# Kernel optimization log

Measured on AMD Instinct MI355X. Metric: run time of the kernel, lower is better.

Reference implementation:

```python
import jax, jax.numpy as jnp
import numpy as np

N = 16384          # num_nodes
B = 2              # batch_size
F = 32             # feature_size (hard-coded in module)
G = 16             # num_gru_units
OUT = 16           # output_dim


def _normalized_laplacian(adj):
    # calculate_laplacian_with_self_loop: D^-1/2 (A + I) D^-1/2
    a = adj + jnp.eye(adj.shape[0], dtype=adj.dtype)
    d = a.sum(axis=1)
    dinv = jax.lax.rsqrt(d)
    return dinv[:, None] * a * dinv[None, :]


def setup_inputs() -> dict:
    key = jax.random.key(0)
    k1, k2, k3, k4 = jax.random.split(key, 4)
    adj = (jax.random.uniform(k1, (N, N), dtype=jnp.float32) < 0.01).astype(jnp.float32)
    laplacian = _normalized_laplacian(adj)
    inputs = jax.random.normal(k2, (B, N, F), dtype=jnp.float32)
    hidden_state = jax.random.normal(k3, (B, N * G), dtype=jnp.float32)
    # xavier_uniform for weights [(G+F), OUT]
    limit = np.sqrt(6.0 / (G + F + OUT)).astype(np.float32)
    weights = jax.random.uniform(k4, (G + F, OUT), dtype=jnp.float32, minval=-limit, maxval=limit)
    biases = jnp.zeros((OUT,), dtype=jnp.float32)
    return {"inputs": inputs, "hidden_state": hidden_state, "laplacian": laplacian,
            "weights": weights, "biases": biases}


def reference(inputs, hidden_state, laplacian, weights, biases):
    b, n, f = inputs.shape
    g = weights.shape[0] - f
    out_dim = weights.shape[1]
    h = hidden_state.reshape(b, n, g)
    cat = jnp.concatenate([inputs, h], axis=2)              # [B, N, F+G]
    # laplacian @ concat over the node dimension (same math as the
    # reshape/transpose dance + per-batch sparse GEMM loop in the original)
    ax = jnp.einsum('mn,bnc->bmc', laplacian, cat)          # [B, N, F+G]
    out = ax @ weights + biases                             # [B, N, OUT]
    return out.reshape(b, n * out_dim)
```

## Files before the change

kernel.cpp:

```cpp
#include <hip/hip_runtime.h>
#include <hip/hip_bf16.h>


#define NN   16384
#define FF   32
#define GG   16
#define OUTD 16
#define C96  96
#define BM   64
#define BK   64
#define SPLITK 4
#define KCHUNK (NN / SPLITK)
#define KITERS (KCHUNK / BK)

typedef __attribute__((ext_vector_type(8))) short short8;
typedef __attribute__((ext_vector_type(4))) float f32x4;

using as1_void = __attribute__((address_space(1))) void;
using as3_void = __attribute__((address_space(3))) void;

__device__ __forceinline__ unsigned short f2bf(float f) {
  __hip_bfloat16 h = __float2bfloat16(f);
  return __builtin_bit_cast(unsigned short, h);
}

__global__ __launch_bounds__(256) void prep_xt(const float* __restrict__ inp,
                                               const float* __restrict__ hid,
                                               unsigned short* __restrict__ xt) {
  __shared__ float lds_cat[C96][64];
  const int tid = threadIdx.x;
  const int n0 = blockIdx.x * 64;

#pragma unroll
  for (int r = 0; r < 2; ++r) {
    int fi = tid + r * 256;
    int n = fi >> 3;
    int f4 = fi & 7;
#pragma unroll
    for (int b = 0; b < 2; ++b) {
      const float4* src = (const float4*)(inp + ((size_t)b * NN + (n0 + n)) * FF) + f4;
      float4 v = *src;
      int c = b * 48 + f4 * 4;
      lds_cat[c + 0][n] = v.x;
      lds_cat[c + 1][n] = v.y;
      lds_cat[c + 2][n] = v.z;
      lds_cat[c + 3][n] = v.w;
    }
  }
  {
    int n = tid >> 2;
    int g4 = tid & 3;
#pragma unroll
    for (int b = 0; b < 2; ++b) {
      const float4* src = (const float4*)(hid + ((size_t)b * NN + (n0 + n)) * GG) + g4;
      float4 v = *src;
      int c = b * 48 + 32 + g4 * 4;
      lds_cat[c + 0][n] = v.x;
      lds_cat[c + 1][n] = v.y;
      lds_cat[c + 2][n] = v.z;
      lds_cat[c + 3][n] = v.w;
    }
  }
  __syncthreads();
#pragma unroll
  for (int r = 0; r < 3; ++r) {
    int u = tid + r * 256;
    int c = u >> 3;
    int nn = (u & 7) * 8;
    short8 o;
#pragma unroll
    for (int j = 0; j < 8; ++j) o[j] = (short)f2bf(lds_cat[c][nn + j]);
    *(short8*)(xt + (size_t)c * NN + n0 + nn) = o;
  }
}

__global__ __launch_bounds__(256, 4) void spmm_main(const float* __restrict__ L,
                                                    const unsigned short* __restrict__ xt,
                                                    float* __restrict__ cp) {
  __shared__ __align__(16) float lds_a[BM * BK];
  __shared__ __align__(16) unsigned short lds_b[C96 * BK];

  const int tid = threadIdx.x;
  const int wave = tid >> 6;
  const int lane = tid & 63;
  const int m0 = blockIdx.x * BM;
  const int kbase = blockIdx.y * KCHUNK;

  const float* asrc[4];
  float* adst[4];
#pragma unroll
  for (int a = 0; a < 4; ++a) {
    int s = wave * 256 + a * 64 + lane;
    int row = s >> 4;
    int cu = (s & 15) ^ (row & 15);
    asrc[a] = L + (size_t)(m0 + row) * NN + kbase + cu * 4;
    adst[a] = lds_a + (wave * 256 + a * 64) * 4;
  }
  const unsigned short* bsrc[3];
  unsigned short* bdst[3];
#pragma unroll
  for (int bi = 0; bi < 3; ++bi) {
    int s = wave * 192 + bi * 64 + lane;
    int c = s >> 3;
    int kg = (s & 7) ^ (c & 7);
    bsrc[bi] = xt + (size_t)c * NN + kbase + kg * 8;
    bdst[bi] = lds_b + (wave * 192 + bi * 64) * 8;
  }

  const int rowA = wave * 16 + (lane & 15);
  const int lq = lane >> 4;
  int aoff[2][2];
#pragma unroll
  for (int kk = 0; kk < 2; ++kk) {
    int cu0 = kk * 8 + lq * 2;
    aoff[kk][0] = (rowA * 16 + (cu0 ^ (rowA & 15))) * 4;
    aoff[kk][1] = (rowA * 16 + ((cu0 + 1) ^ (rowA & 15))) * 4;
  }
  int boff[2][6];
#pragma unroll
  for (int kk = 0; kk < 2; ++kk)
#pragma unroll
    for (int t = 0; t < 6; ++t) {
      int c = t * 16 + (lane & 15);
      int kg = kk * 4 + lq;
      boff[kk][t] = (c * 8 + (kg ^ (c & 7))) * 8;
    }

  f32x4 acc[6];
#pragma unroll
  for (int t = 0; t < 6; ++t) acc[t] = (f32x4){0.f, 0.f, 0.f, 0.f};

  for (int it = 0; it < KITERS; ++it) {
    const int ko = it * BK;
#pragma unroll
    for (int a = 0; a < 4; ++a)
      __builtin_amdgcn_global_load_lds((const as1_void*)(asrc[a] + ko),
                                       (as3_void*)adst[a], 16, 0, 0);
#pragma unroll
    for (int bi = 0; bi < 3; ++bi)
      __builtin_amdgcn_global_load_lds((const as1_void*)(bsrc[bi] + ko),
                                       (as3_void*)bdst[bi], 16, 0, 0);
    __syncthreads();

#pragma unroll
    for (int kk = 0; kk < 2; ++kk) {
      f32x4 a0 = *(const f32x4*)(lds_a + aoff[kk][0]);
      f32x4 a1 = *(const f32x4*)(lds_a + aoff[kk][1]);
      short8 af;
      af[0] = (short)f2bf(a0[0]);
      af[1] = (short)f2bf(a0[1]);
      af[2] = (short)f2bf(a0[2]);
      af[3] = (short)f2bf(a0[3]);
      af[4] = (short)f2bf(a1[0]);
      af[5] = (short)f2bf(a1[1]);
      af[6] = (short)f2bf(a1[2]);
      af[7] = (short)f2bf(a1[3]);
#pragma unroll
      for (int t = 0; t < 6; ++t) {
        short8 bf = *(const short8*)(lds_b + boff[kk][t]);
        acc[t] = __builtin_amdgcn_mfma_f32_16x16x32_bf16(af, bf, acc[t], 0, 0, 0);
      }
    }
    __syncthreads();
  }

  float* cpd = cp + ((size_t)blockIdx.y * NN + m0) * C96;
#pragma unroll
  for (int t = 0; t < 6; ++t) {
    int col = t * 16 + (lane & 15);
#pragma unroll
    for (int r = 0; r < 4; ++r) {
      int row = wave * 16 + lq * 4 + r;
      cpd[(size_t)row * C96 + col] = acc[t][r];
    }
  }
}

__global__ __launch_bounds__(256) void epilogue(const float* __restrict__ cp,
                                                const float* __restrict__ w,
                                                const float* __restrict__ bias,
                                                float* __restrict__ out) {
  __shared__ float lds_c[64 * 97];
  __shared__ float lds_w[48 * 16];
  __shared__ float lds_bias[16];
  const int tid = threadIdx.x;
  const int n0 = blockIdx.x * 64;

  for (int i = tid; i < 768; i += 256) lds_w[i] = w[i];
  if (tid < 16) lds_bias[tid] = bias[tid];

  const size_t base = (size_t)n0 * C96;
#pragma unroll
  for (int i = 0; i < 24; ++i) {
    int e = tid + i * 256;
    float s = 0.f;
#pragma unroll
    for (int sp = 0; sp < 4; ++sp)
      s += cp[(size_t)sp * (NN * C96) + base + e];
    lds_c[e + e / 96] = s;
  }
  __syncthreads();

  const int node = tid >> 2;
  const int b = (tid >> 1) & 1;
  const int o0 = (tid & 1) * 8;
  const float* crow = &lds_c[node * 97 + b * 48];
  float accv[8];
#pragma unroll
  for (int o = 0; o < 8; ++o) accv[o] = lds_bias[o0 + o];
#pragma unroll
  for (int j = 0; j < 48; ++j) {
    float cv = crow[j];
#pragma unroll
    for (int o = 0; o < 8; ++o) accv[o] += cv * lds_w[j * 16 + o0 + o];
  }
  size_t ob = (size_t)b * (NN * OUTD) + (size_t)(n0 + node) * OUTD + o0;
  float4 v0 = {accv[0], accv[1], accv[2], accv[3]};
  float4 v1 = {accv[4], accv[5], accv[6], accv[7]};
  *(float4*)(out + ob) = v0;
  *(float4*)(out + ob + 4) = v1;
}

extern "C" void kernel_launch(void* const* d_in, const int* in_sizes, int n_in,
                              void* d_out, int out_size, void* d_ws, size_t ws_size,
                              hipStream_t stream) {
  (void)in_sizes; (void)n_in; (void)out_size; (void)ws_size;
  const float* inp = (const float*)d_in[0];
  const float* hid = (const float*)d_in[1];
  const float* lap = (const float*)d_in[2];
  const float* wts = (const float*)d_in[3];
  const float* bia = (const float*)d_in[4];
  float* out = (float*)d_out;

  unsigned short* xt = (unsigned short*)d_ws;
  float* cp = (float*)((char*)d_ws + (4u << 20));

  prep_xt<<<NN / 64, 256, 0, stream>>>(inp, hid, xt);
  spmm_main<<<dim3(NN / BM, SPLITK), 256, 0, stream>>>(lap, xt, cp);
  epilogue<<<NN / 64, 256, 0, stream>>>(cp, wts, bia, out);
}
```

Before: 1.343 ms.

## Double-buffer LDS tiles in SpMM main loop and halve split-K with block swizzle

Result: no change. 1.330 ms (-1.0%).

```diff
diff --git a/kernel.cpp b/kernel.cpp
--- a/kernel.cpp
+++ b/kernel.cpp
@@ -9,7 +9,7 @@
 #define C96  96
 #define BM   64
 #define BK   64
-#define SPLITK 4
+#define SPLITK 2
 #define KCHUNK (NN / SPLITK)
 #define KITERS (KCHUNK / BK)
 
@@ -22,6 +22,12 @@
 __device__ __forceinline__ unsigned short f2bf(float f) {
   __hip_bfloat16 h = __float2bfloat16(f);
   return __builtin_bit_cast(unsigned short, h);
+}
+
+__device__ __forceinline__ void wg_barrier() {
+  asm volatile("" ::: "memory");
+  __builtin_amdgcn_s_barrier();
+  asm volatile("" ::: "memory");
 }
 
 __global__ __launch_bounds__(256) void prep_xt(const float* __restrict__ inp,
@@ -74,37 +80,42 @@
   }
 }
 
-__global__ __launch_bounds__(256, 4) void spmm_main(const float* __restrict__ L,
+__global__ __launch_bounds__(256, 2) void spmm_main(const float* __restrict__ L,
                                                     const unsigned short* __restrict__ xt,
                                                     float* __restrict__ cp) {
-  __shared__ __align__(16) float lds_a[BM * BK];
-  __shared__ __align__(16) unsigned short lds_b[C96 * BK];
+  __shared__ __align__(16) float lds_a[2][BM * BK];
+  __shared__ __align__(16) unsigned short lds_b[2][C96 * BK];
 
   const int tid = threadIdx.x;
   const int wave = tid >> 6;
   const int lane = tid & 63;
-  const int m0 = blockIdx.x * BM;
-  const int kbase = blockIdx.y * KCHUNK;
+
+  const int wg = blockIdx.x;
+  const int swz = (wg & 7) * (512 / 8) + (wg >> 3);
+  const int my = swz >> 8;
+  const int mx = swz & 255;
+  const int m0 = mx * BM;
+  const int kbase = my * KCHUNK;
 
   const float* asrc[4];
-  float* adst[4];
+  int adst[4];
 #pragma unroll
   for (int a = 0; a < 4; ++a) {
     int s = wave * 256 + a * 64 + lane;
     int row = s >> 4;
     int cu = (s & 15) ^ (row & 15);
     asrc[a] = L + (size_t)(m0 + row) * NN + kbase + cu * 4;
-    adst[a] = lds_a + (wave * 256 + a * 64) * 4;
+    adst[a] = (wave * 256 + a * 64) * 4;
   }
   const unsigned short* bsrc[3];
-  unsigned short* bdst[3];
+  int bdst[3];
 #pragma unroll
   for (int bi = 0; bi < 3; ++bi) {
     int s = wave * 192 + bi * 64 + lane;
     int c = s >> 3;
     int kg = (s & 7) ^ (c & 7);
     bsrc[bi] = xt + (size_t)c * NN + kbase + kg * 8;
-    bdst[bi] = lds_b + (wave * 192 + bi * 64) * 8;
+    bdst[bi] = (wave * 192 + bi * 64) * 8;
   }
 
   const int rowA = wave * 16 + (lane & 15);
@@ -130,22 +141,22 @@
 #pragma unroll
   for (int t = 0; t < 6; ++t) acc[t] = (f32x4){0.f, 0.f, 0.f, 0.f};
 
-  for (int it = 0; it < KITERS; ++it) {
-    const int ko = it * BK;
+  auto stage = [&](int buf, int ko) {
 #pragma unroll
     for (int a = 0; a < 4; ++a)
       __builtin_amdgcn_global_load_lds((const as1_void*)(asrc[a] + ko),
-                                       (as3_void*)adst[a], 16, 0, 0);
+                                       (as3_void*)(&lds_a[buf][adst[a]]), 16, 0, 0);
 #pragma unroll
     for (int bi = 0; bi < 3; ++bi)
       __builtin_amdgcn_global_load_lds((const as1_void*)(bsrc[bi] + ko),
-                                       (as3_void*)bdst[bi], 16, 0, 0);
-    __syncthreads();
-
+                                       (as3_void*)(&lds_b[buf][bdst[bi]]), 16, 0, 0);
+  };
+
+  auto compute = [&](int buf) {
 #pragma unroll
     for (int kk = 0; kk < 2; ++kk) {
-      f32x4 a0 = *(const f32x4*)(lds_a + aoff[kk][0]);
-      f32x4 a1 = *(const f32x4*)(lds_a + aoff[kk][1]);
+      f32x4 a0 = *(const f32x4*)(&lds_a[buf][aoff[kk][0]]);
+      f32x4 a1 = *(const f32x4*)(&lds_a[buf][aoff[kk][1]]);
       short8 af;
       af[0] = (short)f2bf(a0[0]);
       af[1] = (short)f2bf(a0[1]);
@@ -157,14 +168,29 @@
       af[7] = (short)f2bf(a1[3]);
 #pragma unroll
       for (int t = 0; t < 6; ++t) {
-        short8 bf = *(const short8*)(lds_b + boff[kk][t]);
+        short8 bf = *(const short8*)(&lds_b[buf][boff[kk][t]]);
         acc[t] = __builtin_amdgcn_mfma_f32_16x16x32_bf16(af, bf, acc[t], 0, 0, 0);
       }
     }
-    __syncthreads();
-  }
-
-  float* cpd = cp + ((size_t)blockIdx.y * NN + m0) * C96;
+  };
+
+  stage(0, 0);
+  int cur = 0;
+  for (int it = 0; it < KITERS - 1; ++it) {
+    stage(cur ^ 1, (it + 1) * BK);
+    asm volatile("s_waitcnt vmcnt(7)" ::: "memory");
+    __builtin_amdgcn_s_barrier();
+    asm volatile("" ::: "memory");
+    compute(cur);
+    wg_barrier();
+    cur ^= 1;
+  }
+  asm volatile("s_waitcnt vmcnt(0)" ::: "memory");
+  __builtin_amdgcn_s_barrier();
+  asm volatile("" ::: "memory");
+  compute(cur);
+
+  float* cpd = cp + ((size_t)my * NN + m0) * C96;
 #pragma unroll
   for (int t = 0; t < 6; ++t) {
     int col = t * 16 + (lane & 15);
@@ -195,7 +221,7 @@
     int e = tid + i * 256;
     float s = 0.f;
 #pragma unroll
-    for (int sp = 0; sp < 4; ++sp)
+    for (int sp = 0; sp < SPLITK; ++sp)
       s += cp[(size_t)sp * (NN * C96) + base + e];
     lds_c[e + e / 96] = s;
   }
@@ -236,6 +262,6 @@
   float* cp = (float*)((char*)d_ws + (4u << 20));
 
   prep_xt<<<NN / 64, 256, 0, stream>>>(inp, hid, xt);
-  spmm_main<<<dim3(NN / BM, SPLITK), 256, 0, stream>>>(lap, xt, cp);
+  spmm_main<<<dim3(NN / BM * SPLITK), 256, 0, stream>>>(lap, xt, cp);
   epilogue<<<NN / 64, 256, 0, stream>>>(cp, wts, bia, out);
 }
```

## Load SpMM operands directly from global into registers with prefetch and block swizzle

Applied to the files above, without the earlier changes.

After: 1.533 ms. 14.1% more time.

```diff
diff --git a/kernel.cpp b/kernel.cpp
--- a/kernel.cpp
+++ b/kernel.cpp
@@ -12,12 +12,10 @@
 #define SPLITK 4
 #define KCHUNK (NN / SPLITK)
 #define KITERS (KCHUNK / BK)
+#define NWG   (NN / BM * SPLITK)
 
 typedef __attribute__((ext_vector_type(8))) short short8;
 typedef __attribute__((ext_vector_type(4))) float f32x4;
-
-using as1_void = __attribute__((address_space(1))) void;
-using as3_void = __attribute__((address_space(3))) void;
 
 __device__ __forceinline__ unsigned short f2bf(float f) {
   __hip_bfloat16 h = __float2bfloat16(f);
@@ -77,75 +75,50 @@
 __global__ __launch_bounds__(256, 4) void spmm_main(const float* __restrict__ L,
                                                     const unsigned short* __restrict__ xt,
                                                     float* __restrict__ cp) {
-  __shared__ __align__(16) float lds_a[BM * BK];
-  __shared__ __align__(16) unsigned short lds_b[C96 * BK];
-
   const int tid = threadIdx.x;
   const int wave = tid >> 6;
   const int lane = tid & 63;
-  const int m0 = blockIdx.x * BM;
-  const int kbase = blockIdx.y * KCHUNK;
-
-  const float* asrc[4];
-  float* adst[4];
-#pragma unroll
-  for (int a = 0; a < 4; ++a) {
-    int s = wave * 256 + a * 64 + lane;
-    int row = s >> 4;
-    int cu = (s & 15) ^ (row & 15);
-    asrc[a] = L + (size_t)(m0 + row) * NN + kbase + cu * 4;
-    adst[a] = lds_a + (wave * 256 + a * 64) * 4;
-  }
-  const unsigned short* bsrc[3];
-  unsigned short* bdst[3];
-#pragma unroll
-  for (int bi = 0; bi < 3; ++bi) {
-    int s = wave * 192 + bi * 64 + lane;
-    int c = s >> 3;
-    int kg = (s & 7) ^ (c & 7);
-    bsrc[bi] = xt + (size_t)c * NN + kbase + kg * 8;
-    bdst[bi] = lds_b + (wave * 192 + bi * 64) * 8;
-  }
-
-  const int rowA = wave * 16 + (lane & 15);
   const int lq = lane >> 4;
-  int aoff[2][2];
-#pragma unroll
-  for (int kk = 0; kk < 2; ++kk) {
-    int cu0 = kk * 8 + lq * 2;
-    aoff[kk][0] = (rowA * 16 + (cu0 ^ (rowA & 15))) * 4;
-    aoff[kk][1] = (rowA * 16 + ((cu0 + 1) ^ (rowA & 15))) * 4;
-  }
-  int boff[2][6];
+  const int lr = lane & 15;
+
+  const int wg = blockIdx.x;
+  const int swz = (wg & 7) * (NWG / 8) + (wg >> 3);
+  const int my = swz >> 8;
+  const int mx = swz & 255;
+  const int m0 = mx * BM;
+  const int kbase = my * KCHUNK;
+
+  const float* arow = L + (size_t)(m0 + wave * 16 + lr) * NN + kbase + lq * 8;
+  const unsigned short* bb0 = xt + (size_t)(0 * 16 + lr) * NN + kbase + lq * 8;
+  const unsigned short* bb1 = xt + (size_t)(1 * 16 + lr) * NN + kbase + lq * 8;
+  const unsigned short* bb2 = xt + (size_t)(2 * 16 + lr) * NN + kbase + lq * 8;
+  const unsigned short* bb3 = xt + (size_t)(3 * 16 + lr) * NN + kbase + lq * 8;
+  const unsigned short* bb4 = xt + (size_t)(4 * 16 + lr) * NN + kbase + lq * 8;
+  const unsigned short* bb5 = xt + (size_t)(5 * 16 + lr) * NN + kbase + lq * 8;
+  const unsigned short* bb[6] = {bb0, bb1, bb2, bb3, bb4, bb5};
+
+  f32x4 acc[6];
+#pragma unroll
+  for (int t = 0; t < 6; ++t) acc[t] = (f32x4){0.f, 0.f, 0.f, 0.f};
+
+  f32x4 aC[2][2], aN[2][2];
 #pragma unroll
   for (int kk = 0; kk < 2; ++kk)
 #pragma unroll
-    for (int t = 0; t < 6; ++t) {
-      int c = t * 16 + (lane & 15);
-      int kg = kk * 4 + lq;
-      boff[kk][t] = (c * 8 + (kg ^ (c & 7))) * 8;
-    }
-
-  f32x4 acc[6];
-#pragma unroll
-  for (int t = 0; t < 6; ++t) acc[t] = (f32x4){0.f, 0.f, 0.f, 0.f};
+    for (int j = 0; j < 2; ++j)
+      aC[kk][j] = *(const f32x4*)(arow + kk * 32 + j * 4);
 
   for (int it = 0; it < KITERS; ++it) {
-    const int ko = it * BK;
-#pragma unroll
-    for (int a = 0; a < 4; ++a)
-      __builtin_amdgcn_global_load_lds((const as1_void*)(asrc[a] + ko),
-                                       (as3_void*)adst[a], 16, 0, 0);
-#pragma unroll
-    for (int bi = 0; bi < 3; ++bi)
-      __builtin_amdgcn_global_load_lds((const as1_void*)(bsrc[bi] + ko),
-                                       (as3_void*)bdst[bi], 16, 0, 0);
-    __syncthreads();
+    const int nx = (it + 1 < KITERS) ? (it + 1) : it;
+#pragma unroll
+    for (int kk = 0; kk < 2; ++kk)
+#pragma unroll
+      for (int j = 0; j < 2; ++j)
+        aN[kk][j] = *(const f32x4*)(arow + nx * BK + kk * 32 + j * 4);
 
 #pragma unroll
     for (int kk = 0; kk < 2; ++kk) {
-      f32x4 a0 = *(const f32x4*)(lds_a + aoff[kk][0]);
-      f32x4 a1 = *(const f32x4*)(lds_a + aoff[kk][1]);
+      f32x4 a0 = aC[kk][0], a1 = aC[kk][1];
       short8 af;
       af[0] = (short)f2bf(a0[0]);
       af[1] = (short)f2bf(a0[1]);
@@ -157,17 +130,21 @@
       af[7] = (short)f2bf(a1[3]);
 #pragma unroll
       for (int t = 0; t < 6; ++t) {
-        short8 bf = *(const short8*)(lds_b + boff[kk][t]);
+        short8 bf = *(const short8*)(bb[t] + it * BK + kk * 32);
         acc[t] = __builtin_amdgcn_mfma_f32_16x16x32_bf16(af, bf, acc[t], 0, 0, 0);
       }
     }
-    __syncthreads();
-  }
-
-  float* cpd = cp + ((size_t)blockIdx.y * NN + m0) * C96;
+#pragma unroll
+    for (int kk = 0; kk < 2; ++kk)
+#pragma unroll
+      for (int j = 0; j < 2; ++j)
+        aC[kk][j] = aN[kk][j];
+  }
+
+  float* cpd = cp + ((size_t)my * NN + m0) * C96;
 #pragma unroll
   for (int t = 0; t < 6; ++t) {
-    int col = t * 16 + (lane & 15);
+    int col = t * 16 + lr;
 #pragma unroll
     for (int r = 0; r < 4; ++r) {
       int row = wave * 16 + lq * 4 + r;
@@ -195,7 +172,7 @@
     int e = tid + i * 256;
     float s = 0.f;
 #pragma unroll
-    for (int sp = 0; sp < 4; ++sp)
+    for (int sp = 0; sp < SPLITK; ++sp)
       s += cp[(size_t)sp * (NN * C96) + base + e];
     lds_c[e + e / 96] = s;
   }
@@ -236,6 +213,6 @@
   float* cp = (float*)((char*)d_ws + (4u << 20));
 
   prep_xt<<<NN / 64, 256, 0, stream>>>(inp, hid, xt);
-  spmm_main<<<dim3(NN / BM, SPLITK), 256, 0, stream>>>(lap, xt, cp);
+  spmm_main<<<NWG, 256, 0, stream>>>(lap, xt, cp);
   epilogue<<<NN / 64, 256, 0, stream>>>(cp, wts, bia, out);
 }
```

## Fuse weight projection into SpMM, drop split-K, retile to 32x128

Applied to the files above, without the earlier changes.

Measured after the change: 1.365 ms. No clear change (+1.6%).

```diff
diff --git a/kernel.cpp b/kernel.cpp
--- a/kernel.cpp
+++ b/kernel.cpp
@@ -7,11 +7,10 @@
 #define GG   16
 #define OUTD 16
 #define C96  96
-#define BM   64
-#define BK   64
-#define SPLITK 4
-#define KCHUNK (NN / SPLITK)
-#define KITERS (KCHUNK / BK)
+#define BM   32
+#define BK   128
+#define KITERS (NN / BK)
+#define NWG   (NN / BM)
 
 typedef __attribute__((ext_vector_type(8))) short short8;
 typedef __attribute__((ext_vector_type(4))) float f32x4;
@@ -74,61 +73,74 @@
   }
 }
 
-__global__ __launch_bounds__(256, 4) void spmm_main(const float* __restrict__ L,
-                                                    const unsigned short* __restrict__ xt,
-                                                    float* __restrict__ cp) {
+__global__ __launch_bounds__(256, 2) void spmm_fused(const float* __restrict__ L,
+                                                     const unsigned short* __restrict__ xt,
+                                                     const float* __restrict__ w,
+                                                     const float* __restrict__ bias,
+                                                     float* __restrict__ out) {
   __shared__ __align__(16) float lds_a[BM * BK];
   __shared__ __align__(16) unsigned short lds_b[C96 * BK];
+  __shared__ float lds_w[48 * 16];
+  __shared__ float lds_bias[16];
 
   const int tid = threadIdx.x;
   const int wave = tid >> 6;
   const int lane = tid & 63;
-  const int m0 = blockIdx.x * BM;
-  const int kbase = blockIdx.y * KCHUNK;
+  const int lq = lane >> 4;
+  const int lr = lane & 15;
+  const int chalf = wave & 1;
+  const int rhalf = wave >> 1;
+
+  for (int i = tid; i < 768; i += 256) lds_w[i] = w[i];
+  if (tid < 16) lds_bias[tid] = bias[tid];
+
+  const int wg = blockIdx.x;
+  const int mx = (wg & 7) * (NWG / 8) + (wg >> 3);
+  const int m0 = mx * BM;
 
   const float* asrc[4];
   float* adst[4];
 #pragma unroll
   for (int a = 0; a < 4; ++a) {
-    int s = wave * 256 + a * 64 + lane;
-    int row = s >> 4;
-    int cu = (s & 15) ^ (row & 15);
-    asrc[a] = L + (size_t)(m0 + row) * NN + kbase + cu * 4;
-    adst[a] = lds_a + (wave * 256 + a * 64) * 4;
-  }
-  const unsigned short* bsrc[3];
-  unsigned short* bdst[3];
-#pragma unroll
-  for (int bi = 0; bi < 3; ++bi) {
-    int s = wave * 192 + bi * 64 + lane;
-    int c = s >> 3;
-    int kg = (s & 7) ^ (c & 7);
-    bsrc[bi] = xt + (size_t)c * NN + kbase + kg * 8;
-    bdst[bi] = lds_b + (wave * 192 + bi * 64) * 8;
-  }
-
-  const int rowA = wave * 16 + (lane & 15);
-  const int lq = lane >> 4;
-  int aoff[2][2];
-#pragma unroll
-  for (int kk = 0; kk < 2; ++kk) {
-    int cu0 = kk * 8 + lq * 2;
-    aoff[kk][0] = (rowA * 16 + (cu0 ^ (rowA & 15))) * 4;
-    aoff[kk][1] = (rowA * 16 + ((cu0 + 1) ^ (rowA & 15))) * 4;
-  }
-  int boff[2][6];
-#pragma unroll
-  for (int kk = 0; kk < 2; ++kk)
-#pragma unroll
-    for (int t = 0; t < 6; ++t) {
-      int c = t * 16 + (lane & 15);
+    int s = a * 256 + wave * 64 + lane;
+    int row = s >> 5;
+    int cu = (s & 31) ^ (row & 7);
+    asrc[a] = L + (size_t)(m0 + row) * NN + cu * 4;
+    adst[a] = lds_a + (a * 256 + wave * 64) * 4;
+  }
+  const unsigned short* bsrc[6];
+  unsigned short* bdst[6];
+#pragma unroll
+  for (int bi = 0; bi < 6; ++bi) {
+    int s = bi * 256 + wave * 64 + lane;
+    int c = s >> 4;
+    int kg = (s & 15) ^ (c & 7);
+    bsrc[bi] = xt + (size_t)c * NN + kg * 8;
+    bdst[bi] = lds_b + (bi * 256 + wave * 64) * 8;
+  }
+
+  const int rowA = rhalf * 16 + lr;
+  int aoff[4][2];
+#pragma unroll
+  for (int kk = 0; kk < 4; ++kk)
+#pragma unroll
+    for (int j = 0; j < 2; ++j) {
+      int ug = kk * 8 + lq * 2 + j;
+      aoff[kk][j] = (rowA * 32 + (ug ^ (rowA & 7))) * 4;
+    }
+  int boff[4][3];
+#pragma unroll
+  for (int kk = 0; kk < 4; ++kk)
+#pragma unroll
+    for (int t = 0; t < 3; ++t) {
+      int c = chalf * 48 + t * 16 + lr;
       int kg = kk * 4 + lq;
-      boff[kk][t] = (c * 8 + (kg ^ (c & 7))) * 8;
-    }
-
-  f32x4 acc[6];
-#pragma unroll
-  for (int t = 0; t < 6; ++t) acc[t] = (f32x4){0.f, 0.f, 0.f, 0.f};
+      boff[kk][t] = (c * 16 + (kg ^ (c & 7))) * 8;
+    }
+
+  f32x4 acc[3];
+#pragma unroll
+  for (int t = 0; t < 3; ++t) acc[t] = (f32x4){0.f, 0.f, 0.f, 0.f};
 
   for (int it = 0; it < KITERS; ++it) {
     const int ko = it * BK;
@@ -137,13 +149,13 @@
       __builtin_amdgcn_global_load_lds((const as1_void*)(asrc[a] + ko),
                                        (as3_void*)adst[a], 16, 0, 0);
 #pragma unroll
-    for (int bi = 0; bi < 3; ++bi)
+    for (int bi = 0; bi < 6; ++bi)
       __builtin_amdgcn_global_load_lds((const as1_void*)(bsrc[bi] + ko),
                                        (as3_void*)bdst[bi], 16, 0, 0);
     __syncthreads();
 
 #pragma unroll
-    for (int kk = 0; kk < 2; ++kk) {
+    for (int kk = 0; kk < 4; ++kk) {
       f32x4 a0 = *(const f32x4*)(lds_a + aoff[kk][0]);
       f32x4 a1 = *(const f32x4*)(lds_a + aoff[kk][1]);
       short8 af;
@@ -156,7 +168,7 @@
       af[6] = (short)f2bf(a1[2]);
       af[7] = (short)f2bf(a1[3]);
 #pragma unroll
-      for (int t = 0; t < 6; ++t) {
+      for (int t = 0; t < 3; ++t) {
         short8 bf = *(const short8*)(lds_b + boff[kk][t]);
         acc[t] = __builtin_amdgcn_mfma_f32_16x16x32_bf16(af, bf, acc[t], 0, 0, 0);
       }
@@ -164,61 +176,29 @@
     __syncthreads();
   }
 
-  float* cpd = cp + ((size_t)blockIdx.y * NN + m0) * C96;
-#pragma unroll
-  for (int t = 0; t < 6; ++t) {
-    int col = t * 16 + (lane & 15);
-#pragma unroll
-    for (int r = 0; r < 4; ++r) {
-      int row = wave * 16 + lq * 4 + r;
-      cpd[(size_t)row * C96 + col] = acc[t][r];
-    }
-  }
-}
-
-__global__ __launch_bounds__(256) void epilogue(const float* __restrict__ cp,
-                                                const float* __restrict__ w,
-                                                const float* __restrict__ bias,
-                                                float* __restrict__ out) {
-  __shared__ float lds_c[64 * 97];
-  __shared__ float lds_w[48 * 16];
-  __shared__ float lds_bias[16];
-  const int tid = threadIdx.x;
-  const int n0 = blockIdx.x * 64;
-
-  for (int i = tid; i < 768; i += 256) lds_w[i] = w[i];
-  if (tid < 16) lds_bias[tid] = bias[tid];
-
-  const size_t base = (size_t)n0 * C96;
-#pragma unroll
-  for (int i = 0; i < 24; ++i) {
-    int e = tid + i * 256;
-    float s = 0.f;
-#pragma unroll
-    for (int sp = 0; sp < 4; ++sp)
-      s += cp[(size_t)sp * (NN * C96) + base + e];
-    lds_c[e + e / 96] = s;
-  }
-  __syncthreads();
-
-  const int node = tid >> 2;
-  const int b = (tid >> 1) & 1;
-  const int o0 = (tid & 1) * 8;
-  const float* crow = &lds_c[node * 97 + b * 48];
-  float accv[8];
-#pragma unroll
-  for (int o = 0; o < 8; ++o) accv[o] = lds_bias[o0 + o];
+  float* axl = lds_a + wave * (16 * 49);
+#pragma unroll
+  for (int t = 0; t < 3; ++t) {
+    int col = t * 16 + lr;
+#pragma unroll
+    for (int r = 0; r < 4; ++r)
+      axl[(lq * 4 + r) * 49 + col] = acc[t][r];
+  }
+  const int node = lane >> 2;
+  const int o0 = (lane & 3) * 4;
+  float av[4];
+#pragma unroll
+  for (int o = 0; o < 4; ++o) av[o] = lds_bias[o0 + o];
 #pragma unroll
   for (int j = 0; j < 48; ++j) {
-    float cv = crow[j];
-#pragma unroll
-    for (int o = 0; o < 8; ++o) accv[o] += cv * lds_w[j * 16 + o0 + o];
-  }
-  size_t ob = (size_t)b * (NN * OUTD) + (size_t)(n0 + node) * OUTD + o0;
-  float4 v0 = {accv[0], accv[1], accv[2], accv[3]};
-  float4 v1 = {accv[4], accv[5], accv[6], accv[7]};
-  *(float4*)(out + ob) = v0;
-  *(float4*)(out + ob + 4) = v1;
+    float cv = axl[node * 49 + j];
+#pragma unroll
+    for (int o = 0; o < 4; ++o) av[o] += cv * lds_w[j * 16 + o0 + o];
+  }
+  size_t ob = (size_t)chalf * (NN * OUTD) +
+              (size_t)(m0 + rhalf * 16 + node) * OUTD + o0;
+  float4 v = {av[0], av[1], av[2], av[3]};
+  *(float4*)(out + ob) = v;
 }
 
 extern "C" void kernel_launch(void* const* d_in, const int* in_sizes, int n_in,
@@ -233,9 +213,7 @@
   float* out = (float*)d_out;
 
   unsigned short* xt = (unsigned short*)d_ws;
-  float* cp = (float*)((char*)d_ws + (4u << 20));
 
   prep_xt<<<NN / 64, 256, 0, stream>>>(inp, hid, xt);
-  spmm_main<<<dim3(NN / BM, SPLITK), 256, 0, stream>>>(lap, xt, cp);
-  epilogue<<<NN / 64, 256, 0, stream>>>(cp, wts, bia, out);
-}
+  spmm_fused<<<NWG, 256, 0, stream>>>(lap, xt, wts, bia, out);
+}
```
